# Performance work log

Measured on AMD Instinct MI355X. Metric: run time of the kernel, lower is better.

The kernel has to match this reference:

```python
import jax, jax.numpy as jnp
import numpy as np

DIM = 512
DIM_HEAD = 64
HEADS = 8
DIM_INNER = DIM_HEAD * HEADS
EPS = float(jnp.finfo(jnp.float32).eps)  # torch nn.RMSNorm default eps


def setup_inputs() -> dict:
    key = jax.random.key(0)
    k1, k2, k3, k4 = jax.random.split(key, 4)
    tokens = jax.random.normal(k1, (2, 4096, DIM), dtype=jnp.float32)
    norm_weight = jnp.ones((DIM,), dtype=jnp.float32)
    s = 1.0 / np.sqrt(DIM)
    w_qkv = jax.random.normal(k2, (DIM, 3 * DIM_INNER), dtype=jnp.float32) * s
    w_out = jax.random.normal(k3, (DIM_INNER, DIM), dtype=jnp.float32) * (1.0 / np.sqrt(DIM_INNER))
    return {"tokens": tokens, "norm_weight": norm_weight, "w_qkv": w_qkv, "w_out": w_out}


def reference(tokens, norm_weight, w_qkv, w_out):
    b, n, d = tokens.shape
    scale = DIM_HEAD ** -0.5
    # RMSNorm
    ms = jnp.mean(jnp.square(tokens), axis=-1, keepdims=True)
    x = tokens * jax.lax.rsqrt(ms + EPS) * norm_weight
    # QKV projection, split heads: b n (qkv h d) -> qkv b h n d
    qkv = x @ w_qkv                                   # [b, n, 3*h*dh]
    qkv = qkv.reshape(b, n, 3, HEADS, DIM_HEAD)
    q, k, v = jnp.moveaxis(qkv, 2, 0)                 # each [b, n, h, dh]
    q = jnp.swapaxes(q, 1, 2)                         # [b, h, n, dh]
    k = jnp.swapaxes(k, 1, 2)
    v = jnp.swapaxes(v, 1, 2)
    # naive attention (note: original applies no scale in forward, self.scale unused)
    sim = jnp.einsum('bhid,bhjd->bhij', q, k)
    attn = jax.nn.softmax(sim, axis=-1)
    out = jnp.einsum('bhij,bhjd->bhid', attn, v)
    out = jnp.swapaxes(out, 1, 2).reshape(b, n, DIM_INNER)
    return out @ w_out
```

## Files before the change

### kernel.cpp

```cpp
#include <hip/hip_runtime.h>
#include <stdint.h>
#include <stddef.h>

typedef _Float16 half_t;
typedef __attribute__((ext_vector_type(2))) __fp16 fp16v2;
typedef __attribute__((ext_vector_type(4))) _Float16 f16x4;
typedef __attribute__((ext_vector_type(8))) _Float16 f16x8;
typedef __attribute__((ext_vector_type(4))) float f32x4;

#define EPSF 1.1920928955078125e-07f
#define LOG2E 1.4426950408889634f

#define AS1 __attribute__((address_space(1)))
#define AS3 __attribute__((address_space(3)))

#define WS_XN   0u
#define WS_WQT  4194304u
#define WS_WOT  4980736u
#define WS_Q    5242880u
#define WS_K    9437184u
#define WS_VT   13631488u
#define WS_AO   17825792u
#define WS_NEED_BYTES 44040192u

__device__ __forceinline__ void gload16(const void* g, void* l) {
  __builtin_amdgcn_global_load_lds((const AS1 void*)g, (AS3 void*)l, 16, 0, 0);
}

__device__ __forceinline__ float fast_exp2(float x) {
#if __has_builtin(__builtin_amdgcn_exp2f)
  return __builtin_amdgcn_exp2f(x);
#else
  return exp2f(x);
#endif
}

__global__ __launch_bounds__(256) void k_rmsnorm(const float* __restrict__ t,
                                                 const float* __restrict__ w,
                                                 half_t* __restrict__ xn) {
  int row = blockIdx.x * 4 + (threadIdx.x >> 6);
  int ln = threadIdx.x & 63;
  const float* src = t + (size_t)row * 512 + ln * 8;
  float4 a = *(const float4*)src;
  float4 b = *(const float4*)(src + 4);
  float ss = a.x * a.x + a.y * a.y + a.z * a.z + a.w * a.w
           + b.x * b.x + b.y * b.y + b.z * b.z + b.w * b.w;
#pragma unroll
  for (int m = 32; m >= 1; m >>= 1) ss += __shfl_xor(ss, m);
  float r = rsqrtf(ss * (1.0f / 512.0f) + EPSF);
  const float* wp = w + ln * 8;
  float4 w0 = *(const float4*)wp;
  float4 w1 = *(const float4*)(wp + 4);
  f16x8 o;
  o[0] = (_Float16)(a.x * r * w0.x);
  o[1] = (_Float16)(a.y * r * w0.y);
  o[2] = (_Float16)(a.z * r * w0.z);
  o[3] = (_Float16)(a.w * r * w0.w);
  o[4] = (_Float16)(b.x * r * w1.x);
  o[5] = (_Float16)(b.y * r * w1.y);
  o[6] = (_Float16)(b.z * r * w1.z);
  o[7] = (_Float16)(b.w * r * w1.w);
  *(f16x8*)(xn + (size_t)row * 512 + ln * 8) = o;
}

__global__ __launch_bounds__(256) void k_wtrans(const float* __restrict__ wqkv,
                                                const float* __restrict__ wout,
                                                half_t* __restrict__ wqt,
                                                half_t* __restrict__ wot) {
  __shared__ half_t tile[64][65];
  int b = blockIdx.x;
  const float* src; half_t* dst; int N, tk, tn;
  if (b < 192) { src = wqkv; dst = wqt; N = 1536; tk = b / 24; tn = b - tk * 24; }
  else { b -= 192; src = wout; dst = wot; N = 512; tk = b >> 3; tn = b & 7; }
  int c = threadIdx.x & 63;
  int r0 = threadIdx.x >> 6;
#pragma unroll
  for (int i = 0; i < 16; ++i) {
    int r = i * 4 + r0;
    tile[r][c] = (_Float16)src[(size_t)(tk * 64 + r) * N + tn * 64 + c];
  }
  __syncthreads();
#pragma unroll
  for (int i = 0; i < 16; ++i) {
    int n = i * 4 + r0;
    dst[(size_t)(tn * 64 + n) * 512 + tk * 64 + c] = tile[c][n];
  }
}

__device__ __forceinline__ void gemm_core(const half_t* __restrict__ A,
                                          const half_t* __restrict__ Bt,
                                          int m0, int n0, int Ksz,
                                          half_t* Al, half_t* Bl,
                                          f32x4 acc[4][4]) {
  int wv = threadIdx.x >> 6, ln = threadIdx.x & 63;
  int wm = (wv >> 1) << 6, wn = (wv & 1) << 6;
  for (int kt = 0; kt < Ksz; kt += 64) {
#pragma unroll
    for (int i = 0; i < 4; ++i) {
      int seg = wv * 4 + i;
      int r = seg * 8 + (ln >> 3);
      int cb = ((ln & 7) * 16) ^ ((r & 7) << 4);
      gload16((const char*)(A + (size_t)(m0 + r) * Ksz + kt) + cb, (char*)Al + seg * 1024);
      gload16((const char*)(Bt + (size_t)(n0 + r) * Ksz + kt) + cb, (char*)Bl + seg * 1024);
    }
    __syncthreads();
#pragma unroll
    for (int kc = 0; kc < 2; ++kc) {
      f16x8 af[4], bf[4];
#pragma unroll
      for (int mt = 0; mt < 4; ++mt) {
        int rr = wm + mt * 16 + (ln & 15);
        af[mt] = *(const f16x8*)((const char*)Al + rr * 128 +
                                 ((kc * 64 + (ln >> 4) * 16) ^ ((rr & 7) << 4)));
      }
#pragma unroll
      for (int nt = 0; nt < 4; ++nt) {
        int rr = wn + nt * 16 + (ln & 15);
        bf[nt] = *(const f16x8*)((const char*)Bl + rr * 128 +
                                 ((kc * 64 + (ln >> 4) * 16) ^ ((rr & 7) << 4)));
      }
#pragma unroll
      for (int mt = 0; mt < 4; ++mt)
#pragma unroll
        for (int nt = 0; nt < 4; ++nt)
          acc[mt][nt] = __builtin_amdgcn_mfma_f32_16x16x32_f16(af[mt], bf[nt], acc[mt][nt], 0, 0, 0);
    }
    __syncthreads();
  }
}

__global__ __launch_bounds__(256, 2) void k_gemm_qkv(const half_t* __restrict__ A,
                                                     const half_t* __restrict__ Bt,
                                                     half_t* __restrict__ q,
                                                     half_t* __restrict__ kk,
                                                     half_t* __restrict__ vt) {
  __shared__ __align__(16) half_t Al[128 * 64];
  __shared__ __align__(16) half_t Bl[128 * 64];
  f32x4 acc[4][4];
  f32x4 z = {0.f, 0.f, 0.f, 0.f};
#pragma unroll
  for (int i = 0; i < 4; ++i)
#pragma unroll
    for (int j = 0; j < 4; ++j) acc[i][j] = z;
  int m0 = blockIdx.x * 128, n0 = blockIdx.y * 128;
  gemm_core(A, Bt, m0, n0, 512, Al, Bl, acc);
  int wv = threadIdx.x >> 6, ln = threadIdx.x & 63;
  int wm = (wv >> 1) << 6, wn = (wv & 1) << 6;
#pragma unroll
  for (int mt = 0; mt < 4; ++mt) {
#pragma unroll
    for (int nt = 0; nt < 4; ++nt) {
      int gn = n0 + wn + nt * 16 + (ln & 15);
      int qkv_i = gn >> 9;
      int h = (gn >> 6) & 7;
      int d = gn & 63;
#pragma unroll
      for (int j = 0; j < 4; ++j) {
        int gm = m0 + wm + mt * 16 + (ln >> 4) * 4 + j;
        int head = ((gm >> 12) << 3) | h;
        int n = gm & 4095;
        float av = acc[mt][nt][j];
        if (qkv_i == 0)      q [((size_t)head * 4096 + n) * 64 + d] = (_Float16)(av * LOG2E);
        else if (qkv_i == 1) kk[((size_t)head * 4096 + n) * 64 + d] = (_Float16)av;
        else {
          int pcol = (n & ~31) | (((n >> 2) & 3) << 3) | (((n >> 4) & 1) << 2) | (n & 3);
          vt[((size_t)head * 64 + d) * 4096 + pcol] = (_Float16)av;
        }
      }
    }
  }
}

__global__ __launch_bounds__(256, 2) void k_gemm_out(const half_t* __restrict__ A,
                                                     const half_t* __restrict__ Bt,
                                                     float* __restrict__ out) {
  __shared__ __align__(16) half_t Al[128 * 64];
  __shared__ __align__(16) half_t Bl[128 * 64];
  f32x4 acc[4][4];
  f32x4 z = {0.f, 0.f, 0.f, 0.f};
#pragma unroll
  for (int i = 0; i < 4; ++i)
#pragma unroll
    for (int j = 0; j < 4; ++j) acc[i][j] = z;
  int m0 = blockIdx.x * 128, n0 = blockIdx.y * 128;
  gemm_core(A, Bt, m0, n0, 512, Al, Bl, acc);
  int wv = threadIdx.x >> 6, ln = threadIdx.x & 63;
  int wm = (wv >> 1) << 6, wn = (wv & 1) << 6;
#pragma unroll
  for (int mt = 0; mt < 4; ++mt)
#pragma unroll
    for (int nt = 0; nt < 4; ++nt) {
      int gn = n0 + wn + nt * 16 + (ln & 15);
#pragma unroll
      for (int j = 0; j < 4; ++j) {
        int gm = m0 + wm + mt * 16 + (ln >> 4) * 4 + j;
        out[(size_t)gm * 512 + gn] = acc[mt][nt][j];
      }
    }
}

__global__ __launch_bounds__(512, 4) void k_attn(const half_t* __restrict__ q,
                                                 const half_t* __restrict__ kg,
                                                 const half_t* __restrict__ vt,
                                                 half_t* __restrict__ ao) {
  __shared__ __align__(16) char lds[32768];
  const int wv = threadIdx.x >> 6, ln = threadIdx.x & 63;
  const int bid = blockIdx.x;
  const int lin = (bid & 7) * 64 + (bid >> 3);
  const int head = lin >> 5;
  const int qt = lin & 31;
  const int q0 = qt * 128 + wv * 16;
  const char* qh = (const char*)(q  + (size_t)head * 4096 * 64);
  const char* kh = (const char*)(kg + (size_t)head * 4096 * 64);
  const char* vh = (const char*)(vt + (size_t)head * 64 * 4096);

  f16x8 qf[2];
#pragma unroll
  for (int kc = 0; kc < 2; ++kc) {
    int r = q0 + (ln & 15);
    qf[kc] = *(const f16x8*)(qh + (size_t)r * 128 + kc * 64 + (ln >> 4) * 16);
  }

  const int sr = wv * 8 + (ln >> 3);
  const int cb = ((ln & 7) * 16) ^ ((sr & 7) << 4);
  const char* ks = kh + (size_t)sr * 128 + cb;
  const char* vs = vh + (size_t)sr * 8192 + cb;
  const int lo = wv * 1024;

  float mrun = 0.0f;
  f32x4 oacc[4];
  f32x4 lacc;
  const f32x4 z = {0.f, 0.f, 0.f, 0.f};
  lacc = z;
#pragma unroll
  for (int dt = 0; dt < 4; ++dt) oacc[dt] = z;
  f16x8 ones;
#pragma unroll
  for (int e = 0; e < 8; ++e) ones[e] = (_Float16)1.0f;

  gload16(ks, lds + lo);
  gload16(vs, lds + 8192 + lo);
  ks += 8192; vs += 128;
  __syncthreads();

  int cur = 0;
#pragma unroll 1
  for (int t = 0; t < 64; ++t) {
    if (t < 63) {
      char* base = lds + (cur ^ 1) * 16384;
      gload16(ks, base + lo);
      gload16(vs, base + 8192 + lo);
      ks += 8192; vs += 128;
    }
    const char* Kb = lds + cur * 16384;
    const char* Vb = Kb + 8192;

    f32x4 s[4];
    {
      float nm = -mrun;
      f32x4 mi = {nm, nm, nm, nm};
      s[0] = mi; s[1] = mi; s[2] = mi; s[3] = mi;
    }
    __builtin_amdgcn_s_setprio(1);
#pragma unroll
    for (int kc = 0; kc < 2; ++kc) {
      f16x8 kf[4];
#pragma unroll
      for (int kt = 0; kt < 4; ++kt) {
        int rr = kt * 16 + (ln & 15);
        kf[kt] = *(const f16x8*)(Kb + rr * 128 + ((kc * 64 + (ln >> 4) * 16) ^ ((rr & 7) << 4)));
      }
#pragma unroll
      for (int kt = 0; kt < 4; ++kt)
        s[kt] = __builtin_amdgcn_mfma_f32_16x16x32_f16(kf[kt], qf[kc], s[kt], 0, 0, 0);
    }
    __builtin_amdgcn_s_setprio(0);

    f16x8 vf[2][4];
#pragma unroll
    for (int dt = 0; dt < 4; ++dt) {
      int rr = dt * 16 + (ln & 15);
      int sw = (rr & 7) << 4;
      vf[0][dt] = *(const f16x8*)(Vb + rr * 128 + (((ln >> 4) * 16) ^ sw));
      vf[1][dt] = *(const f16x8*)(Vb + rr * 128 + ((64 + (ln >> 4) * 16) ^ sw));
    }

    f16x8 pf[2];
    {
      float m0 = fmaxf(fmaxf(s[0][0], s[0][1]), s[0][2]);
      float m1 = fmaxf(fmaxf(s[0][3], s[1][0]), s[1][1]);
      float m2 = fmaxf(fmaxf(s[1][2], s[1][3]), s[2][0]);
      float m3 = fmaxf(fmaxf(s[2][1], s[2][2]), s[2][3]);
      float m4 = fmaxf(fmaxf(s[3][0], s[3][1]), s[3][2]);
      float m5 = fmaxf(fmaxf(m0, m1), m2);
      float m6 = fmaxf(fmaxf(m3, m4), s[3][3]);
      float tm = fmaxf(m5, m6);
      tm = fmaxf(tm, __shfl_xor(tm, 16));
      tm = fmaxf(tm, __shfl_xor(tm, 32));
      float p[4][4];
      if (__builtin_expect(__any(tm > 11.0f), 0)) {
        float dlt = fmaxf(tm, 0.0f);
        float sc = fast_exp2(-dlt);
        mrun += dlt;
        lacc[0] *= sc;
#pragma unroll
        for (int dt = 0; dt < 4; ++dt) {
          oacc[dt][0] *= sc; oacc[dt][1] *= sc;
          oacc[dt][2] *= sc; oacc[dt][3] *= sc;
        }
#pragma unroll
        for (int kt = 0; kt < 4; ++kt)
#pragma unroll
          for (int r = 0; r < 4; ++r) p[kt][r] = fast_exp2(s[kt][r] - dlt);
      } else {
#pragma unroll
        for (int kt = 0; kt < 4; ++kt)
#pragma unroll
          for (int r = 0; r < 4; ++r) p[kt][r] = fast_exp2(s[kt][r]);
      }
#pragma unroll
      for (int kc = 0; kc < 2; ++kc) {
        union { f16x8 v; fp16v2 h[4]; } u;
        u.h[0] = __builtin_amdgcn_cvt_pkrtz(p[2 * kc][0], p[2 * kc][1]);
        u.h[1] = __builtin_amdgcn_cvt_pkrtz(p[2 * kc][2], p[2 * kc][3]);
        u.h[2] = __builtin_amdgcn_cvt_pkrtz(p[2 * kc + 1][0], p[2 * kc + 1][1]);
        u.h[3] = __builtin_amdgcn_cvt_pkrtz(p[2 * kc + 1][2], p[2 * kc + 1][3]);
        pf[kc] = u.v;
      }
    }

    __builtin_amdgcn_s_setprio(1);
#pragma unroll
    for (int dt = 0; dt < 4; ++dt)
      oacc[dt] = __builtin_amdgcn_mfma_f32_16x16x32_f16(vf[0][dt], pf[0], oacc[dt], 0, 0, 0);
    lacc = __builtin_amdgcn_mfma_f32_16x16x32_f16(ones, pf[0], lacc, 0, 0, 0);
#pragma unroll
    for (int dt = 0; dt < 4; ++dt)
      oacc[dt] = __builtin_amdgcn_mfma_f32_16x16x32_f16(vf[1][dt], pf[1], oacc[dt], 0, 0, 0);
    lacc = __builtin_amdgcn_mfma_f32_16x16x32_f16(ones, pf[1], lacc, 0, 0, 0);
    __builtin_amdgcn_s_setprio(0);

    __syncthreads();
    cur ^= 1;
  }

  const int b = head >> 3, h = head & 7;
  {
    float inv = 1.0f / lacc[0];
    int n = q0 + (ln & 15);
    half_t* dst = ao + ((size_t)(b * 4096 + n)) * 512 + h * 64 + (ln >> 4) * 4;
#pragma unroll
    for (int dt = 0; dt < 4; ++dt) {
      f16x4 o4;
      o4[0] = (_Float16)(oacc[dt][0] * inv);
      o4[1] = (_Float16)(oacc[dt][1] * inv);
      o4[2] = (_Float16)(oacc[dt][2] * inv);
      o4[3] = (_Float16)(oacc[dt][3] * inv);
      *(f16x4*)(dst + dt * 16) = o4;
    }
  }
}

extern "C" void kernel_launch(void* const* d_in, const int* in_sizes, int n_in,
                              void* d_out, int out_size, void* d_ws, size_t ws_size,
                              hipStream_t stream) {
  if (ws_size < WS_NEED_BYTES) return;
  const float* tokens = (const float*)d_in[0];
  const float* nw     = (const float*)d_in[1];
  const float* wqkv   = (const float*)d_in[2];
  const float* wout   = (const float*)d_in[3];
  float* out = (float*)d_out;
  half_t* ws = (half_t*)d_ws;
  half_t* xn  = ws + WS_XN;
  half_t* wqt = ws + WS_WQT;
  half_t* wot = ws + WS_WOT;
  half_t* qb  = ws + WS_Q;
  half_t* kb  = ws + WS_K;
  half_t* vtb = ws + WS_VT;
  half_t* aob = ws + WS_AO;

  k_rmsnorm<<<2048, 256, 0, stream>>>(tokens, nw, xn);
  k_wtrans<<<256, 256, 0, stream>>>(wqkv, wout, wqt, wot);
  k_gemm_qkv<<<dim3(64, 12), 256, 0, stream>>>(xn, wqt, qb, kb, vtb);
  k_attn<<<512, 512, 0, stream>>>(qb, kb, vtb, aob);
  k_gemm_out<<<dim3(64, 4), 256, 0, stream>>>(aob, wot, out);
}
```

Baseline: 134.0 us.

## Switch attention to 32x32x16 MFMA with 32 query rows per wave

The attention kernel now uses 32x32x16 MFMA instructions instead of 16x16x32, so each wave handles 32 query rows and each block covers 256 queries, which halves the grid. The V-transpose permutation written by the QKV GEMM is changed to match the new MFMA operand layout. The larger tile reuses each K/V tile loaded into LDS across twice as many queries and cuts the number of cross-lane max shuffles. In exchange, accumulator register pressure grows, occupancy drops to 2 blocks per CU, and only 256 blocks are launched, which may underfill the GPU.

```diff
diff --git a/kernel.cpp b/kernel.cpp
--- a/kernel.cpp
+++ b/kernel.cpp
@@ -7,6 +7,7 @@
 typedef __attribute__((ext_vector_type(4))) _Float16 f16x4;
 typedef __attribute__((ext_vector_type(8))) _Float16 f16x8;
 typedef __attribute__((ext_vector_type(4))) float f32x4;
+typedef __attribute__((ext_vector_type(16))) float f32x16;
 
 #define EPSF 1.1920928955078125e-07f
 #define LOG2E 1.4426950408889634f
@@ -163,7 +164,7 @@
         if (qkv_i == 0)      q [((size_t)head * 4096 + n) * 64 + d] = (_Float16)(av * LOG2E);
         else if (qkv_i == 1) kk[((size_t)head * 4096 + n) * 64 + d] = (_Float16)av;
         else {
-          int pcol = (n & ~31) | (((n >> 2) & 3) << 3) | (((n >> 4) & 1) << 2) | (n & 3);
+          int pcol = (n & ~12) | ((n & 4) << 1) | ((n & 8) >> 1);
           vt[((size_t)head * 64 + d) * 4096 + pcol] = (_Float16)av;
         }
       }
@@ -199,26 +200,28 @@
     }
 }
 
-__global__ __launch_bounds__(512, 4) void k_attn(const half_t* __restrict__ q,
+__global__ __launch_bounds__(512, 2) void k_attn(const half_t* __restrict__ q,
                                                  const half_t* __restrict__ kg,
                                                  const half_t* __restrict__ vt,
                                                  half_t* __restrict__ ao) {
   __shared__ __align__(16) char lds[32768];
   const int wv = threadIdx.x >> 6, ln = threadIdx.x & 63;
+  const int hi = ln >> 5;
   const int bid = blockIdx.x;
-  const int lin = (bid & 7) * 64 + (bid >> 3);
-  const int head = lin >> 5;
-  const int qt = lin & 31;
-  const int q0 = qt * 128 + wv * 16;
+  const int lin = (bid & 7) * 32 + (bid >> 3);
+  const int head = lin >> 4;
+  const int qt = lin & 15;
+  const int q0 = qt * 256 + wv * 32;
   const char* qh = (const char*)(q  + (size_t)head * 4096 * 64);
   const char* kh = (const char*)(kg + (size_t)head * 4096 * 64);
   const char* vh = (const char*)(vt + (size_t)head * 64 * 4096);
 
-  f16x8 qf[2];
-#pragma unroll
-  for (int kc = 0; kc < 2; ++kc) {
-    int r = q0 + (ln & 15);
-    qf[kc] = *(const f16x8*)(qh + (size_t)r * 128 + kc * 64 + (ln >> 4) * 16);
+  f16x8 qf[4];
+  {
+    int r = q0 + (ln & 31);
+#pragma unroll
+    for (int kt = 0; kt < 4; ++kt)
+      qf[kt] = *(const f16x8*)(qh + (size_t)r * 128 + kt * 32 + hi * 16);
   }
 
   const int sr = wv * 8 + (ln >> 3);
@@ -227,13 +230,18 @@
   const char* vs = vh + (size_t)sr * 8192 + cb;
   const int lo = wv * 1024;
 
+  const int rbase = (ln & 31) * 128;
+  const int sw = (ln & 7) << 4;
+  int colx[4];
+#pragma unroll
+  for (int kt = 0; kt < 4; ++kt) colx[kt] = (kt * 32 + hi * 16) ^ sw;
+
   float mrun = 0.0f;
-  f32x4 oacc[4];
-  f32x4 lacc;
-  const f32x4 z = {0.f, 0.f, 0.f, 0.f};
-  lacc = z;
-#pragma unroll
-  for (int dt = 0; dt < 4; ++dt) oacc[dt] = z;
+  f32x16 oacc[2];
+  f32x16 lacc;
+  const f32x16 z16 = {0.f,0.f,0.f,0.f,0.f,0.f,0.f,0.f,0.f,0.f,0.f,0.f,0.f,0.f,0.f,0.f};
+  lacc = z16;
+  oacc[0] = z16; oacc[1] = z16;
   f16x8 ones;
 #pragma unroll
   for (int e = 0; e < 8; ++e) ones[e] = (_Float16)1.0f;
@@ -255,109 +263,102 @@
     const char* Kb = lds + cur * 16384;
     const char* Vb = Kb + 8192;
 
-    f32x4 s[4];
+    f32x16 s0, s1;
     {
       float nm = -mrun;
-      f32x4 mi = {nm, nm, nm, nm};
-      s[0] = mi; s[1] = mi; s[2] = mi; s[3] = mi;
+      f32x16 mi = {nm,nm,nm,nm,nm,nm,nm,nm,nm,nm,nm,nm,nm,nm,nm,nm};
+      s0 = mi; s1 = mi;
     }
     __builtin_amdgcn_s_setprio(1);
 #pragma unroll
-    for (int kc = 0; kc < 2; ++kc) {
-      f16x8 kf[4];
-#pragma unroll
-      for (int kt = 0; kt < 4; ++kt) {
-        int rr = kt * 16 + (ln & 15);
-        kf[kt] = *(const f16x8*)(Kb + rr * 128 + ((kc * 64 + (ln >> 4) * 16) ^ ((rr & 7) << 4)));
-      }
-#pragma unroll
-      for (int kt = 0; kt < 4; ++kt)
-        s[kt] = __builtin_amdgcn_mfma_f32_16x16x32_f16(kf[kt], qf[kc], s[kt], 0, 0, 0);
+    for (int kt = 0; kt < 4; ++kt) {
+      f16x8 kf0 = *(const f16x8*)(Kb + rbase + colx[kt]);
+      f16x8 kf1 = *(const f16x8*)(Kb + 4096 + rbase + colx[kt]);
+      s0 = __builtin_amdgcn_mfma_f32_32x32x16_f16(kf0, qf[kt], s0, 0, 0, 0);
+      s1 = __builtin_amdgcn_mfma_f32_32x32x16_f16(kf1, qf[kt], s1, 0, 0, 0);
     }
     __builtin_amdgcn_s_setprio(0);
 
     f16x8 vf[2][4];
 #pragma unroll
-    for (int dt = 0; dt < 4; ++dt) {
-      int rr = dt * 16 + (ln & 15);
-      int sw = (rr & 7) << 4;
-      vf[0][dt] = *(const f16x8*)(Vb + rr * 128 + (((ln >> 4) * 16) ^ sw));
-      vf[1][dt] = *(const f16x8*)(Vb + rr * 128 + ((64 + (ln >> 4) * 16) ^ sw));
-    }
-
-    f16x8 pf[2];
+    for (int km = 0; km < 4; ++km) {
+      vf[0][km] = *(const f16x8*)(Vb + rbase + colx[km]);
+      vf[1][km] = *(const f16x8*)(Vb + 4096 + rbase + colx[km]);
+    }
+
+    f16x8 pf[4];
     {
-      float m0 = fmaxf(fmaxf(s[0][0], s[0][1]), s[0][2]);
-      float m1 = fmaxf(fmaxf(s[0][3], s[1][0]), s[1][1]);
-      float m2 = fmaxf(fmaxf(s[1][2], s[1][3]), s[2][0]);
-      float m3 = fmaxf(fmaxf(s[2][1], s[2][2]), s[2][3]);
-      float m4 = fmaxf(fmaxf(s[3][0], s[3][1]), s[3][2]);
-      float m5 = fmaxf(fmaxf(m0, m1), m2);
-      float m6 = fmaxf(fmaxf(m3, m4), s[3][3]);
-      float tm = fmaxf(m5, m6);
-      tm = fmaxf(tm, __shfl_xor(tm, 16));
-      tm = fmaxf(tm, __shfl_xor(tm, 32));
-      float p[4][4];
+      float a0 = fmaxf(fmaxf(s0[0], s0[1]), s0[2]);
+      float a1 = fmaxf(fmaxf(s0[3], s0[4]), s0[5]);
+      float a2 = fmaxf(fmaxf(s0[6], s0[7]), s0[8]);
+      float a3 = fmaxf(fmaxf(s0[9], s0[10]), s0[11]);
+      float a4 = fmaxf(fmaxf(s0[12], s0[13]), s0[14]);
+      float a5 = fmaxf(fmaxf(s0[15], s1[0]), s1[1]);
+      float a6 = fmaxf(fmaxf(s1[2], s1[3]), s1[4]);
+      float a7 = fmaxf(fmaxf(s1[5], s1[6]), s1[7]);
+      float a8 = fmaxf(fmaxf(s1[8], s1[9]), s1[10]);
+      float a9 = fmaxf(fmaxf(s1[11], s1[12]), s1[13]);
+      float b0 = fmaxf(fmaxf(a0, a1), a2);
+      float b1 = fmaxf(fmaxf(a3, a4), a5);
+      float b2 = fmaxf(fmaxf(a6, a7), a8);
+      float b3 = fmaxf(fmaxf(a9, s1[14]), s1[15]);
+      float tm = fmaxf(fmaxf(b0, b1), fmaxf(b2, b3));
       if (__builtin_expect(__any(tm > 11.0f), 0)) {
+        tm = fmaxf(tm, __shfl_xor(tm, 32));
         float dlt = fmaxf(tm, 0.0f);
         float sc = fast_exp2(-dlt);
         mrun += dlt;
         lacc[0] *= sc;
 #pragma unroll
-        for (int dt = 0; dt < 4; ++dt) {
-          oacc[dt][0] *= sc; oacc[dt][1] *= sc;
-          oacc[dt][2] *= sc; oacc[dt][3] *= sc;
-        }
-#pragma unroll
-        for (int kt = 0; kt < 4; ++kt)
-#pragma unroll
-          for (int r = 0; r < 4; ++r) p[kt][r] = fast_exp2(s[kt][r] - dlt);
+        for (int e = 0; e < 16; ++e) { oacc[0][e] *= sc; oacc[1][e] *= sc; }
+#pragma unroll
+        for (int e = 0; e < 16; ++e) { s0[e] = fast_exp2(s0[e] - dlt); s1[e] = fast_exp2(s1[e] - dlt); }
       } else {
 #pragma unroll
-        for (int kt = 0; kt < 4; ++kt)
-#pragma unroll
-          for (int r = 0; r < 4; ++r) p[kt][r] = fast_exp2(s[kt][r]);
-      }
-#pragma unroll
-      for (int kc = 0; kc < 2; ++kc) {
+        for (int e = 0; e < 16; ++e) { s0[e] = fast_exp2(s0[e]); s1[e] = fast_exp2(s1[e]); }
+      }
+#pragma unroll
+      for (int km = 0; km < 4; ++km) {
+        const f32x16& sv = (km < 2) ? s0 : s1;
+        int o = (km & 1) * 8;
         union { f16x8 v; fp16v2 h[4]; } u;
-        u.h[0] = __builtin_amdgcn_cvt_pkrtz(p[2 * kc][0], p[2 * kc][1]);
-        u.h[1] = __builtin_amdgcn_cvt_pkrtz(p[2 * kc][2], p[2 * kc][3]);
-        u.h[2] = __builtin_amdgcn_cvt_pkrtz(p[2 * kc + 1][0], p[2 * kc + 1][1]);
-        u.h[3] = __builtin_amdgcn_cvt_pkrtz(p[2 * kc + 1][2], p[2 * kc + 1][3]);
-        pf[kc] = u.v;
+        u.h[0] = __builtin_amdgcn_cvt_pkrtz(sv[o + 0], sv[o + 1]);
+        u.h[1] = __builtin_amdgcn_cvt_pkrtz(sv[o + 2], sv[o + 3]);
+        u.h[2] = __builtin_amdgcn_cvt_pkrtz(sv[o + 4], sv[o + 5]);
+        u.h[3] = __builtin_amdgcn_cvt_pkrtz(sv[o + 6], sv[o + 7]);
+        pf[km] = u.v;
       }
     }
 
     __builtin_amdgcn_s_setprio(1);
 #pragma unroll
-    for (int dt = 0; dt < 4; ++dt)
-      oacc[dt] = __builtin_amdgcn_mfma_f32_16x16x32_f16(vf[0][dt], pf[0], oacc[dt], 0, 0, 0);
-    lacc = __builtin_amdgcn_mfma_f32_16x16x32_f16(ones, pf[0], lacc, 0, 0, 0);
-#pragma unroll
-    for (int dt = 0; dt < 4; ++dt)
-      oacc[dt] = __builtin_amdgcn_mfma_f32_16x16x32_f16(vf[1][dt], pf[1], oacc[dt], 0, 0, 0);
-    lacc = __builtin_amdgcn_mfma_f32_16x16x32_f16(ones, pf[1], lacc, 0, 0, 0);
+    for (int km = 0; km < 4; ++km) {
+      oacc[0] = __builtin_amdgcn_mfma_f32_32x32x16_f16(vf[0][km], pf[km], oacc[0], 0, 0, 0);
+      oacc[1] = __builtin_amdgcn_mfma_f32_32x32x16_f16(vf[1][km], pf[km], oacc[1], 0, 0, 0);
+      lacc    = __builtin_amdgcn_mfma_f32_32x32x16_f16(ones,     pf[km], lacc,    0, 0, 0);
+    }
     __builtin_amdgcn_s_setprio(0);
 
     __syncthreads();
     cur ^= 1;
   }
 
-  const int b = head >> 3, h = head & 7;
+  const int bb = head >> 3, h = head & 7;
   {
     float inv = 1.0f / lacc[0];
-    int n = q0 + (ln & 15);
-    half_t* dst = ao + ((size_t)(b * 4096 + n)) * 512 + h * 64 + (ln >> 4) * 4;
-#pragma unroll
-    for (int dt = 0; dt < 4; ++dt) {
-      f16x4 o4;
-      o4[0] = (_Float16)(oacc[dt][0] * inv);
-      o4[1] = (_Float16)(oacc[dt][1] * inv);
-      o4[2] = (_Float16)(oacc[dt][2] * inv);
-      o4[3] = (_Float16)(oacc[dt][3] * inv);
-      *(f16x4*)(dst + dt * 16) = o4;
-    }
+    int n = q0 + (ln & 31);
+    half_t* dst = ao + ((size_t)(bb * 4096 + n)) * 512 + h * 64;
+#pragma unroll
+    for (int db = 0; db < 2; ++db)
+#pragma unroll
+      for (int a = 0; a < 4; ++a) {
+        f16x4 o4;
+        o4[0] = (_Float16)(oacc[db][a * 4 + 0] * inv);
+        o4[1] = (_Float16)(oacc[db][a * 4 + 1] * inv);
+        o4[2] = (_Float16)(oacc[db][a * 4 + 2] * inv);
+        o4[3] = (_Float16)(oacc[db][a * 4 + 3] * inv);
+        *(f16x4*)(dst + db * 32 + a * 8 + hi * 4) = o4;
+      }
   }
 }
 
@@ -382,6 +383,6 @@
   k_rmsnorm<<<2048, 256, 0, stream>>>(tokens, nw, xn);
   k_wtrans<<<256, 256, 0, stream>>>(wqkv, wout, wqt, wot);
   k_gemm_qkv<<<dim3(64, 12), 256, 0, stream>>>(xn, wqt, qb, kb, vtb);
-  k_attn<<<512, 512, 0, stream>>>(qb, kb, vtb, aob);
+  k_attn<<<256, 512, 0, stream>>>(qb, kb, vtb, aob);
   k_gemm_out<<<dim3(64, 4), 256, 0, stream>>>(aob, wot, out);
 }
```

Measured after the change: 140.2 us. +4.7%, slower.
